# Kernel tuning notes

Measured on AMD Instinct MI355X. Metric: run time of the kernel, lower is better.

Reference implementation:

```python
import jax, jax.numpy as jnp
import numpy as np

B, L, H = 32, 1024, 1024  # kv_length must equal hidden_size for the bmm to typecheck


def setup_inputs() -> dict:
    key = jax.random.key(0)
    ks = jax.random.split(key, 9)
    s = 0.02  # small init so tanh does not saturate
    return {
        "query": jax.random.normal(ks[0], (B, L, H), dtype=jnp.float32),
        "key": jax.random.normal(ks[1], (B, L, H), dtype=jnp.float32),
        "value": jax.random.normal(ks[2], (B, L, H), dtype=jnp.float32),
        "w1_w": jax.random.normal(ks[3], (H, H), dtype=jnp.float32) * s,
        "w1_b": jax.random.normal(ks[4], (H,), dtype=jnp.float32) * s,
        "w2_w": jax.random.normal(ks[5], (H, H), dtype=jnp.float32) * s,
        "w2_b": jax.random.normal(ks[6], (H,), dtype=jnp.float32) * s,
        "v_w": jax.random.normal(ks[7], (H, H), dtype=jnp.float32) * s,
        "v_b": jax.random.normal(ks[8], (H,), dtype=jnp.float32) * s,
    }


def reference(query, key, value, w1_w, w1_b, w2_w, w2_b, v_w, v_b):
    # score_fn: v(tanh(w1(query) + w2(value))); `key` is unused (del key in source)
    h = jnp.tanh(jnp.einsum("blh,oh->blo", query, w1_w) + w1_b
                 + jnp.einsum("blh,oh->blo", value, w2_w) + w2_b)  # (B, L, H)
    score = jnp.einsum("blh,oh->blo", h, v_w) + v_b                 # (B, L, H)
    attention_weights = jax.nn.softmax(score, axis=-1)              # (B, L, H)
    # torch.bmm(weights, value): contracts weights' last dim (H) with value's kv dim (==H)
    context_vector = jnp.einsum("blk,bkh->blh", attention_weights, value)
    return (attention_weights, context_vector)
```

## Files before the change

### kernel.cpp

```cpp
#include <hip/hip_runtime.h>
#include <cstdint>

using u16 = unsigned short;
using u32 = unsigned int;
typedef __attribute__((ext_vector_type(4))) float f32x4;
typedef __attribute__((ext_vector_type(8))) short short8;
typedef __attribute__((ext_vector_type(4))) u16 u16x4;

__device__ __forceinline__ u16 f2bf(float f) {
  u32 u = __builtin_bit_cast(u32, f);
  u += 0x7FFFu + ((u >> 16) & 1u);
  return (u16)(u >> 16);
}

__device__ __forceinline__ void gload16(const void* g, void* l) {
  __builtin_amdgcn_global_load_lds(
      (const __attribute__((address_space(1))) void*)g,
      (__attribute__((address_space(3))) void*)l, 16, 0, 0);
}

__device__ __forceinline__ float fast_tanh(float x) {
  float ax = fabsf(x);
  float e = __expf(-2.0f * ax);
  float r = (1.0f - e) / (1.0f + e);
  return x < 0.0f ? -r : r;
}

__device__ __forceinline__ void swz_mn(int bid, int& m0, int& n0) {
  int swz = (bid & 7) * 256 + (bid >> 3);
  n0 = (swz & 7) << 7;
  m0 = (swz >> 3) << 7;
}

__global__ void cvt_ker(const float4* __restrict__ src, u16x4* __restrict__ dst, int n4) {
  int i = blockIdx.x * 256 + threadIdx.x;
  if (i < n4) {
    float4 f = src[i];
    u16x4 o = { f2bf(f.x), f2bf(f.y), f2bf(f.z), f2bf(f.w) };
    dst[i] = o;
  }
}

__device__ __forceinline__ void gemm_tile_acc(
    const u16* __restrict__ A, const u16* __restrict__ B,
    int K, int lda, int ldb, int m0, int n0,
    u16* As, u16* Bs, f32x4 acc[4][4])
{
  const int tid = threadIdx.x;
  const int w = tid >> 6, lane = tid & 63;
  const int wr = w >> 1, wc = w & 1;
  const int lr = lane & 15, kg = (lane >> 4) << 3;

  for (int k0 = 0; k0 < K; k0 += 32) {
    __syncthreads();
    #pragma unroll
    for (int i = 0; i < 2; i++) {
      int idx = i * 2048 + w * 512 + lane * 8;
      int r = idx >> 5, c = idx & 31;
      gload16(A + (size_t)(m0 + r) * lda + (k0 + c), As + (i * 2048 + w * 512));
      gload16(B + (size_t)(n0 + r) * ldb + (k0 + c), Bs + (i * 2048 + w * 512));
    }
    __syncthreads();

    short8 a[4], b[4];
    #pragma unroll
    for (int mi = 0; mi < 4; mi++)
      a[mi] = *(const short8*)&As[(wr * 64 + mi * 16 + lr) * 32 + kg];
    #pragma unroll
    for (int ni = 0; ni < 4; ni++)
      b[ni] = *(const short8*)&Bs[(wc * 64 + ni * 16 + lr) * 32 + kg];
    #pragma unroll
    for (int mi = 0; mi < 4; mi++)
      #pragma unroll
      for (int ni = 0; ni < 4; ni++)
        acc[mi][ni] = __builtin_amdgcn_mfma_f32_16x16x32_bf16(a[mi], b[ni], acc[mi][ni], 0, 0, 0);
  }
}

__global__ void gemm1_ker(const u16* __restrict__ q, const u16* __restrict__ v,
                          const u16* __restrict__ w1, const u16* __restrict__ w2,
                          const float* __restrict__ b1, const float* __restrict__ b2,
                          u16* __restrict__ H)
{
  __shared__ u16 As[4096], Bs[4096];
  int m0, n0;
  swz_mn(blockIdx.x, m0, n0);
  f32x4 acc[4][4];
  #pragma unroll
  for (int mi = 0; mi < 4; mi++)
    #pragma unroll
    for (int ni = 0; ni < 4; ni++) acc[mi][ni] = (f32x4){0.f, 0.f, 0.f, 0.f};

  gemm_tile_acc(q, w1, 1024, 1024, 1024, m0, n0, As, Bs, acc);
  gemm_tile_acc(v, w2, 1024, 1024, 1024, m0, n0, As, Bs, acc);

  int tid = threadIdx.x, w = tid >> 6, lane = tid & 63;
  int wr = w >> 1, wc = w & 1, lr = lane & 15, hi = lane >> 4;
  #pragma unroll
  for (int ni = 0; ni < 4; ni++) {
    int col = n0 + wc * 64 + ni * 16 + lr;
    float bias = b1[col] + b2[col];
    #pragma unroll
    for (int mi = 0; mi < 4; mi++) {
      #pragma unroll
      for (int r = 0; r < 4; r++) {
        int row = m0 + wr * 64 + mi * 16 + hi * 4 + r;
        H[(size_t)row * 1024 + col] = f2bf(fast_tanh(acc[mi][ni][r] + bias));
      }
    }
  }
}

__global__ void gemm2_ker(const u16* __restrict__ h, const u16* __restrict__ vw,
                          const float* __restrict__ vb, float* __restrict__ score)
{
  __shared__ u16 As[4096], Bs[4096];
  int m0, n0;
  swz_mn(blockIdx.x, m0, n0);
  f32x4 acc[4][4];
  #pragma unroll
  for (int mi = 0; mi < 4; mi++)
    #pragma unroll
    for (int ni = 0; ni < 4; ni++) acc[mi][ni] = (f32x4){0.f, 0.f, 0.f, 0.f};

  gemm_tile_acc(h, vw, 1024, 1024, 1024, m0, n0, As, Bs, acc);

  int tid = threadIdx.x, w = tid >> 6, lane = tid & 63;
  int wr = w >> 1, wc = w & 1, lr = lane & 15, hi = lane >> 4;
  #pragma unroll
  for (int ni = 0; ni < 4; ni++) {
    int col = n0 + wc * 64 + ni * 16 + lr;
    float bias = vb[col];
    #pragma unroll
    for (int mi = 0; mi < 4; mi++) {
      #pragma unroll
      for (int r = 0; r < 4; r++) {
        int row = m0 + wr * 64 + mi * 16 + hi * 4 + r;
        score[(size_t)row * 1024 + col] = acc[mi][ni][r] + bias;
      }
    }
  }
}

__global__ void transpose_ker(const u16* __restrict__ in, u16* __restrict__ out) {
  __shared__ u16 tile[64][68];
  int b = blockIdx.z;
  int h0 = blockIdx.x * 64, l0 = blockIdx.y * 64;
  const u16* src = in + (size_t)b * 1048576;
  u16* dst = out + (size_t)b * 1048576;
  int t = threadIdx.x;
  #pragma unroll
  for (int i = 0; i < 4; i++) {
    int idx = i * 1024 + t * 4;
    int r = idx >> 6, c = idx & 63;
    *(u16x4*)&tile[r][c] = *(const u16x4*)&src[(size_t)(l0 + r) * 1024 + h0 + c];
  }
  __syncthreads();
  #pragma unroll
  for (int i = 0; i < 4; i++) {
    int idx = i * 1024 + t * 4;
    int hr = idx >> 6, lc = idx & 63;
    u16x4 val = { tile[lc][hr], tile[lc + 1][hr], tile[lc + 2][hr], tile[lc + 3][hr] };
    *(u16x4*)&dst[(size_t)(h0 + hr) * 1024 + l0 + lc] = val;
  }
}

__global__ void softmax_ker(float* __restrict__ sc, u16* __restrict__ wbf) {
  int tid = threadIdx.x;
  int w = tid >> 6, lane = tid & 63;
  size_t row = (size_t)blockIdx.x * 4 + w;
  float* p = sc + row * 1024;
  float4 v[4];
  float mx = -3.4e38f;
  #pragma unroll
  for (int c = 0; c < 4; c++) {
    v[c] = *(const float4*)&p[c * 256 + lane * 4];
    mx = fmaxf(mx, fmaxf(fmaxf(v[c].x, v[c].y), fmaxf(v[c].z, v[c].w)));
  }
  #pragma unroll
  for (int s = 32; s; s >>= 1) mx = fmaxf(mx, __shfl_xor(mx, s, 64));
  float sum = 0.f;
  #pragma unroll
  for (int c = 0; c < 4; c++) {
    v[c].x = __expf(v[c].x - mx); v[c].y = __expf(v[c].y - mx);
    v[c].z = __expf(v[c].z - mx); v[c].w = __expf(v[c].w - mx);
    sum += v[c].x + v[c].y + v[c].z + v[c].w;
  }
  #pragma unroll
  for (int s = 32; s; s >>= 1) sum += __shfl_xor(sum, s, 64);
  float inv = 1.0f / sum;
  #pragma unroll
  for (int c = 0; c < 4; c++) {
    float4 o;
    o.x = v[c].x * inv; o.y = v[c].y * inv; o.z = v[c].z * inv; o.w = v[c].w * inv;
    *(float4*)&p[c * 256 + lane * 4] = o;
    u16x4 ob = { f2bf(o.x), f2bf(o.y), f2bf(o.z), f2bf(o.w) };
    *(u16x4*)&wbf[row * 1024 + c * 256 + lane * 4] = ob;
  }
}

__global__ void gemm3_ker(const u16* __restrict__ wbf, const u16* __restrict__ vT,
                          float* __restrict__ ctx)
{
  __shared__ u16 As[4096], Bs[4096];
  int m0, n0;
  swz_mn(blockIdx.x, m0, n0);
  const u16* Bb = vT + (size_t)(m0 >> 10) * 1048576;
  f32x4 acc[4][4];
  #pragma unroll
  for (int mi = 0; mi < 4; mi++)
    #pragma unroll
    for (int ni = 0; ni < 4; ni++) acc[mi][ni] = (f32x4){0.f, 0.f, 0.f, 0.f};

  gemm_tile_acc(wbf, Bb, 1024, 1024, 1024, m0, n0, As, Bs, acc);

  int tid = threadIdx.x, w = tid >> 6, lane = tid & 63;
  int wr = w >> 1, wc = w & 1, lr = lane & 15, hi = lane >> 4;
  #pragma unroll
  for (int ni = 0; ni < 4; ni++) {
    int col = n0 + wc * 64 + ni * 16 + lr;
    #pragma unroll
    for (int mi = 0; mi < 4; mi++) {
      #pragma unroll
      for (int r = 0; r < 4; r++) {
        int row = m0 + wr * 64 + mi * 16 + hi * 4 + r;
        ctx[(size_t)row * 1024 + col] = acc[mi][ni][r];
      }
    }
  }
}

extern "C" void kernel_launch(void* const* d_in, const int* in_sizes, int n_in,
                              void* d_out, int out_size, void* d_ws, size_t ws_size,
                              hipStream_t stream) {
  const float* q   = (const float*)d_in[0];
  const float* v   = (const float*)d_in[2];
  const float* w1w = (const float*)d_in[3];
  const float* b1  = (const float*)d_in[4];
  const float* w2w = (const float*)d_in[5];
  const float* b2  = (const float*)d_in[6];
  const float* vww = (const float*)d_in[7];
  const float* vb  = (const float*)d_in[8];

  float* out_w = (float*)d_out;
  float* out_c = out_w + (size_t)33554432;

  u16* q_bf  = (u16*)d_ws;
  u16* v_bf  = q_bf + 33554432;
  u16* h_bf  = v_bf + 33554432;
  u16* w1_bf = h_bf + 33554432;
  u16* w2_bf = w1_bf + 1048576;
  u16* vw_bf = w2_bf + 1048576;
  u16* wsm_bf = q_bf;
  u16* vT_bf  = h_bf;

  if (ws_size < (size_t)207618048) return;

  cvt_ker<<<32768, 256, 0, stream>>>((const float4*)q,   (u16x4*)q_bf,  8388608);
  cvt_ker<<<32768, 256, 0, stream>>>((const float4*)v,   (u16x4*)v_bf,  8388608);
  cvt_ker<<<1024,  256, 0, stream>>>((const float4*)w1w, (u16x4*)w1_bf, 262144);
  cvt_ker<<<1024,  256, 0, stream>>>((const float4*)w2w, (u16x4*)w2_bf, 262144);
  cvt_ker<<<1024,  256, 0, stream>>>((const float4*)vww, (u16x4*)vw_bf, 262144);

  gemm1_ker<<<2048, 256, 0, stream>>>(q_bf, v_bf, w1_bf, w2_bf, b1, b2, h_bf);
  gemm2_ker<<<2048, 256, 0, stream>>>(h_bf, vw_bf, vb, out_w);
  transpose_ker<<<dim3(16, 16, 32), 256, 0, stream>>>(v_bf, vT_bf);
  softmax_ker<<<8192, 256, 0, stream>>>(out_w, wsm_bf);
  gemm3_ker<<<2048, 256, 0, stream>>>(wsm_bf, vT_bf, out_c);
}
```

Measured before the change: 548.2 us.

## Rewrite GEMMs as 256x256-tile, 8-wave double-buffered pipelined kernels with swizzled LDS

Replaces the simple 128x128 GEMM loop, which synchronised twice per 32-wide K step, with a 256x256-tile, 512-thread kernel. The new loop stages 64-wide K tiles into double-buffered LDS several sub-steps ahead using direct global-to-LDS loads with explicit vmcnt waits. It adds an XOR-swizzled LDS layout against bank conflicts, s_setprio around the MFMA bursts, and a fused two-GEMM K loop for gemm1. The aim is to raise data reuse and overlap memory traffic with MFMA work, at the cost of 128KB of LDS per block, heavy register pressure, and fragile hand-tuned wait counts.

```diff
diff --git a/kernel.cpp b/kernel.cpp
--- a/kernel.cpp
+++ b/kernel.cpp
@@ -26,10 +26,14 @@
   return x < 0.0f ? -r : r;
 }
 
-__device__ __forceinline__ void swz_mn(int bid, int& m0, int& n0) {
-  int swz = (bid & 7) * 256 + (bid >> 3);
-  n0 = (swz & 7) << 7;
-  m0 = (swz >> 3) << 7;
+#define SBAR() do { asm volatile("" ::: "memory"); __builtin_amdgcn_s_barrier(); asm volatile("" ::: "memory"); } while (0)
+
+__device__ __forceinline__ int swz(int L) { return L ^ (((L >> 9) & 1) << 5); }
+
+__device__ __forceinline__ void swz_mn256(int bid, int& m0, int& n0) {
+  int s = (bid & 7) * 64 + (bid >> 3);
+  n0 = (s & 3) << 8;
+  m0 = (s >> 2) << 8;
 }
 
 __global__ void cvt_ker(const float4* __restrict__ src, u16x4* __restrict__ dst, int n4) {
@@ -41,101 +45,163 @@
   }
 }
 
-__device__ __forceinline__ void gemm_tile_acc(
-    const u16* __restrict__ A, const u16* __restrict__ B,
-    int K, int lda, int ldb, int m0, int n0,
-    u16* As, u16* Bs, f32x4 acc[4][4])
+__device__ __forceinline__ void stage_half(
+    const u16* __restrict__ A0, const u16* __restrict__ B0,
+    const u16* __restrict__ A1, const u16* __restrict__ B1,
+    int half_nt, u16* lds, int j, int m0, int n0, int w, int rc0, int rc1)
+{
+  int jt = j >> 2, hh = j & 3;
+  int kk = hh >> 1, isA = hh & 1;
+  const u16* src;
+  int kt;
+  if (jt < half_nt) { src = isA ? A0 : B0; kt = jt; }
+  else              { src = isA ? A1 : B1; kt = jt - half_nt; }
+  int base_row = isA ? m0 : n0;
+  int koff = kt * 64 + kk * 32;
+  u16* dst = lds + ((jt & 1) * 4 + hh) * 8192 + w * 512;
+  const u16* g0 = src + (size_t)base_row * 1024 + koff;
+  gload16(g0 + rc0, dst);
+  gload16(g0 + rc1, dst + 4096);
+}
+
+__device__ __forceinline__ void gemm8p_loop(
+    const u16* __restrict__ A0, const u16* __restrict__ B0,
+    const u16* __restrict__ A1, const u16* __restrict__ B1,
+    int half_nt, int NT, int m0, int n0, u16* lds, f32x4 acc[8][4])
 {
   const int tid = threadIdx.x;
   const int w = tid >> 6, lane = tid & 63;
-  const int wr = w >> 1, wc = w & 1;
-  const int lr = lane & 15, kg = (lane >> 4) << 3;
-
-  for (int k0 = 0; k0 < K; k0 += 32) {
-    __syncthreads();
-    #pragma unroll
-    for (int i = 0; i < 2; i++) {
-      int idx = i * 2048 + w * 512 + lane * 8;
-      int r = idx >> 5, c = idx & 31;
-      gload16(A + (size_t)(m0 + r) * lda + (k0 + c), As + (i * 2048 + w * 512));
-      gload16(B + (size_t)(n0 + r) * ldb + (k0 + c), Bs + (i * 2048 + w * 512));
+  const int wr = w >> 2, wc = w & 3;
+  const int lr = lane & 15, g = lane >> 4;
+
+  int rc0, rc1;
+  {
+    int seg0 = w * 64 + lane, seg1 = 512 + w * 64 + lane;
+    int L0 = swz(seg0 * 16), L1 = swz(seg1 * 16);
+    rc0 = (L0 >> 6) * 1024 + ((L0 & 63) >> 1);
+    rc1 = (L1 >> 6) * 1024 + ((L1 & 63) >> 1);
+  }
+  int aoff[8], boff[4];
+  #pragma unroll
+  for (int mi = 0; mi < 8; mi++)
+    aoff[mi] = swz((wr * 128 + mi * 16 + lr) * 64 + g * 16);
+  #pragma unroll
+  for (int ni = 0; ni < 4; ni++)
+    boff[ni] = swz((wc * 64 + ni * 16 + lr) * 64 + g * 16);
+
+  #pragma unroll
+  for (int j = 0; j < 4; j++)
+    stage_half(A0, B0, A1, B1, half_nt, lds, j, m0, n0, w, rc0, rc1);
+  asm volatile("s_waitcnt vmcnt(4)" ::: "memory");
+  #pragma unroll
+  for (int j = 4; j < 7; j++)
+    stage_half(A0, B0, A1, B1, half_nt, lds, j, m0, n0, w, rc0, rc1);
+  asm volatile("s_waitcnt vmcnt(6)" ::: "memory");
+  SBAR();
+
+  for (int t = 0; t < NT; ++t) {
+    const int buf = t & 1;
+    short8 bb0, bb1, bb2, bb3;
+    #pragma unroll
+    for (int p = 0; p < 4; ++p) {
+      const int kk = p >> 1, mh = p & 1;
+      const char* halfA = (const char*)(lds + (buf * 4 + 1 + kk * 2) * 8192);
+      const char* halfB = (const char*)(lds + (buf * 4 + kk * 2) * 8192);
+      if (mh == 0) {
+        bb0 = *(const short8*)(halfB + boff[0]);
+        bb1 = *(const short8*)(halfB + boff[1]);
+        bb2 = *(const short8*)(halfB + boff[2]);
+        bb3 = *(const short8*)(halfB + boff[3]);
+      }
+      short8 a0 = *(const short8*)(halfA + aoff[mh * 4 + 0]);
+      short8 a1 = *(const short8*)(halfA + aoff[mh * 4 + 1]);
+      short8 a2 = *(const short8*)(halfA + aoff[mh * 4 + 2]);
+      short8 a3 = *(const short8*)(halfA + aoff[mh * 4 + 3]);
+
+      int j = t * 4 + p + 7;
+      if (j < NT * 4)
+        stage_half(A0, B0, A1, B1, half_nt, lds, j, m0, n0, w, rc0, rc1);
+
+      SBAR();
+      __builtin_amdgcn_s_setprio(1);
+      #pragma unroll
+      for (int ni = 0; ni < 4; ni++) {
+        short8 b = ni == 0 ? bb0 : ni == 1 ? bb1 : ni == 2 ? bb2 : bb3;
+        acc[mh * 4 + 0][ni] = __builtin_amdgcn_mfma_f32_16x16x32_bf16(a0, b, acc[mh * 4 + 0][ni], 0, 0, 0);
+        acc[mh * 4 + 1][ni] = __builtin_amdgcn_mfma_f32_16x16x32_bf16(a1, b, acc[mh * 4 + 1][ni], 0, 0, 0);
+        acc[mh * 4 + 2][ni] = __builtin_amdgcn_mfma_f32_16x16x32_bf16(a2, b, acc[mh * 4 + 2][ni], 0, 0, 0);
+        acc[mh * 4 + 3][ni] = __builtin_amdgcn_mfma_f32_16x16x32_bf16(a3, b, acc[mh * 4 + 3][ni], 0, 0, 0);
+      }
+      __builtin_amdgcn_s_setprio(0);
+      if (p == 3 && t < NT - 1) {
+        if (t == NT - 2) asm volatile("s_waitcnt vmcnt(0)" ::: "memory");
+        else             asm volatile("s_waitcnt vmcnt(6)" ::: "memory");
+      }
+      SBAR();
     }
-    __syncthreads();
-
-    short8 a[4], b[4];
-    #pragma unroll
-    for (int mi = 0; mi < 4; mi++)
-      a[mi] = *(const short8*)&As[(wr * 64 + mi * 16 + lr) * 32 + kg];
-    #pragma unroll
-    for (int ni = 0; ni < 4; ni++)
-      b[ni] = *(const short8*)&Bs[(wc * 64 + ni * 16 + lr) * 32 + kg];
-    #pragma unroll
-    for (int mi = 0; mi < 4; mi++)
-      #pragma unroll
-      for (int ni = 0; ni < 4; ni++)
-        acc[mi][ni] = __builtin_amdgcn_mfma_f32_16x16x32_bf16(a[mi], b[ni], acc[mi][ni], 0, 0, 0);
-  }
-}
-
-__global__ void gemm1_ker(const u16* __restrict__ q, const u16* __restrict__ v,
-                          const u16* __restrict__ w1, const u16* __restrict__ w2,
-                          const float* __restrict__ b1, const float* __restrict__ b2,
-                          u16* __restrict__ H)
-{
-  __shared__ u16 As[4096], Bs[4096];
+  }
+}
+
+__global__ void __launch_bounds__(512, 2)
+gemm1_ker(const u16* __restrict__ q, const u16* __restrict__ v,
+          const u16* __restrict__ w1, const u16* __restrict__ w2,
+          const float* __restrict__ b1, const float* __restrict__ b2,
+          u16* __restrict__ H)
+{
+  __shared__ u16 lds[65536];
   int m0, n0;
-  swz_mn(blockIdx.x, m0, n0);
-  f32x4 acc[4][4];
-  #pragma unroll
-  for (int mi = 0; mi < 4; mi++)
+  swz_mn256(blockIdx.x, m0, n0);
+  f32x4 acc[8][4];
+  #pragma unroll
+  for (int mi = 0; mi < 8; mi++)
     #pragma unroll
     for (int ni = 0; ni < 4; ni++) acc[mi][ni] = (f32x4){0.f, 0.f, 0.f, 0.f};
 
-  gemm_tile_acc(q, w1, 1024, 1024, 1024, m0, n0, As, Bs, acc);
-  gemm_tile_acc(v, w2, 1024, 1024, 1024, m0, n0, As, Bs, acc);
+  gemm8p_loop(q, w1, v, w2, 16, 32, m0, n0, lds, acc);
 
   int tid = threadIdx.x, w = tid >> 6, lane = tid & 63;
-  int wr = w >> 1, wc = w & 1, lr = lane & 15, hi = lane >> 4;
+  int wr = w >> 2, wc = w & 3, lr = lane & 15, g = lane >> 4;
   #pragma unroll
   for (int ni = 0; ni < 4; ni++) {
     int col = n0 + wc * 64 + ni * 16 + lr;
     float bias = b1[col] + b2[col];
     #pragma unroll
-    for (int mi = 0; mi < 4; mi++) {
+    for (int mi = 0; mi < 8; mi++) {
       #pragma unroll
       for (int r = 0; r < 4; r++) {
-        int row = m0 + wr * 64 + mi * 16 + hi * 4 + r;
+        int row = m0 + wr * 128 + mi * 16 + g * 4 + r;
         H[(size_t)row * 1024 + col] = f2bf(fast_tanh(acc[mi][ni][r] + bias));
       }
     }
   }
 }
 
-__global__ void gemm2_ker(const u16* __restrict__ h, const u16* __restrict__ vw,
-                          const float* __restrict__ vb, float* __restrict__ score)
-{
-  __shared__ u16 As[4096], Bs[4096];
+__global__ void __launch_bounds__(512, 2)
+gemm2_ker(const u16* __restrict__ h, const u16* __restrict__ vw,
+          const float* __restrict__ vb, float* __restrict__ score)
+{
+  __shared__ u16 lds[65536];
   int m0, n0;
-  swz_mn(blockIdx.x, m0, n0);
-  f32x4 acc[4][4];
-  #pragma unroll
-  for (int mi = 0; mi < 4; mi++)
+  swz_mn256(blockIdx.x, m0, n0);
+  f32x4 acc[8][4];
+  #pragma unroll
+  for (int mi = 0; mi < 8; mi++)
     #pragma unroll
     for (int ni = 0; ni < 4; ni++) acc[mi][ni] = (f32x4){0.f, 0.f, 0.f, 0.f};
 
-  gemm_tile_acc(h, vw, 1024, 1024, 1024, m0, n0, As, Bs, acc);
+  gemm8p_loop(h, vw, h, vw, 16, 16, m0, n0, lds, acc);
 
   int tid = threadIdx.x, w = tid >> 6, lane = tid & 63;
-  int wr = w >> 1, wc = w & 1, lr = lane & 15, hi = lane >> 4;
+  int wr = w >> 2, wc = w & 3, lr = lane & 15, g = lane >> 4;
   #pragma unroll
   for (int ni = 0; ni < 4; ni++) {
     int col = n0 + wc * 64 + ni * 16 + lr;
     float bias = vb[col];
     #pragma unroll
-    for (int mi = 0; mi < 4; mi++) {
+    for (int mi = 0; mi < 8; mi++) {
       #pragma unroll
       for (int r = 0; r < 4; r++) {
-        int row = m0 + wr * 64 + mi * 16 + hi * 4 + r;
+        int row = m0 + wr * 128 + mi * 16 + g * 4 + r;
         score[(size_t)row * 1024 + col] = acc[mi][ni][r] + bias;
       }
     }
@@ -199,31 +265,32 @@
   }
 }
 
-__global__ void gemm3_ker(const u16* __restrict__ wbf, const u16* __restrict__ vT,
-                          float* __restrict__ ctx)
-{
-  __shared__ u16 As[4096], Bs[4096];
+__global__ void __launch_bounds__(512, 2)
+gemm3_ker(const u16* __restrict__ wbf, const u16* __restrict__ vT,
+          float* __restrict__ ctx)
+{
+  __shared__ u16 lds[65536];
   int m0, n0;
-  swz_mn(blockIdx.x, m0, n0);
+  swz_mn256(blockIdx.x, m0, n0);
   const u16* Bb = vT + (size_t)(m0 >> 10) * 1048576;
-  f32x4 acc[4][4];
-  #pragma unroll
-  for (int mi = 0; mi < 4; mi++)
+  f32x4 acc[8][4];
+  #pragma unroll
+  for (int mi = 0; mi < 8; mi++)
     #pragma unroll
     for (int ni = 0; ni < 4; ni++) acc[mi][ni] = (f32x4){0.f, 0.f, 0.f, 0.f};
 
-  gemm_tile_acc(wbf, Bb, 1024, 1024, 1024, m0, n0, As, Bs, acc);
+  gemm8p_loop(wbf, Bb, wbf, Bb, 16, 16, m0, n0, lds, acc);
 
   int tid = threadIdx.x, w = tid >> 6, lane = tid & 63;
-  int wr = w >> 1, wc = w & 1, lr = lane & 15, hi = lane >> 4;
+  int wr = w >> 2, wc = w & 3, lr = lane & 15, g = lane >> 4;
   #pragma unroll
   for (int ni = 0; ni < 4; ni++) {
     int col = n0 + wc * 64 + ni * 16 + lr;
     #pragma unroll
-    for (int mi = 0; mi < 4; mi++) {
+    for (int mi = 0; mi < 8; mi++) {
       #pragma unroll
       for (int r = 0; r < 4; r++) {
-        int row = m0 + wr * 64 + mi * 16 + hi * 4 + r;
+        int row = m0 + wr * 128 + mi * 16 + g * 4 + r;
         ctx[(size_t)row * 1024 + col] = acc[mi][ni][r];
       }
     }
@@ -262,9 +329,9 @@
   cvt_ker<<<1024,  256, 0, stream>>>((const float4*)w2w, (u16x4*)w2_bf, 262144);
   cvt_ker<<<1024,  256, 0, stream>>>((const float4*)vww, (u16x4*)vw_bf, 262144);
 
-  gemm1_ker<<<2048, 256, 0, stream>>>(q_bf, v_bf, w1_bf, w2_bf, b1, b2, h_bf);
-  gemm2_ker<<<2048, 256, 0, stream>>>(h_bf, vw_bf, vb, out_w);
+  gemm1_ker<<<512, 512, 0, stream>>>(q_bf, v_bf, w1_bf, w2_bf, b1, b2, h_bf);
+  gemm2_ker<<<512, 512, 0, stream>>>(h_bf, vw_bf, vb, out_w);
   transpose_ker<<<dim3(16, 16, 32), 256, 0, stream>>>(v_bf, vT_bf);
   softmax_ker<<<8192, 256, 0, stream>>>(out_w, wsm_bf);
-  gemm3_ker<<<2048, 256, 0, stream>>>(wsm_bf, vT_bf, out_c);
-}
+  gemm3_ker<<<512, 512, 0, stream>>>(wsm_bf, vT_bf, out_c);
+}
```

New measurement: 491.0 us. 10.4% less time.
